# Kernel tuning notes

Measured on AMD Instinct MI355X. Metric: run time of the kernel, lower is better.

## Reference

```python
import jax, jax.numpy as jnp
import numpy as np

TOP_N = 2
NUM_GATES = 8
EPS = 1e-9
THRESHOLD = 0.2          # threshold_train for the 2nd expert
CAPACITY_FACTOR = 1.25   # capacity_factor_train (training mode)
MIN_EXPERT_CAPACITY = 4


def setup_inputs() -> dict:
    key = jax.random.key(0)
    k1, k2, k3 = jax.random.split(key, 3)
    b, n, dim = 4, 2048, 1024
    x = jax.random.normal(k1, (b, n, dim), jnp.float32)
    W_g = jax.random.normal(k2, (NUM_GATES, dim), jnp.float32) * 0.02
    # replaces torch.zeros_like(gates).uniform_(0,1) inside forward
    probs = jax.random.uniform(k3, (TOP_N, b, n), jnp.float32)
    return {"x": x, "W_g": W_g, "probs": probs}


def reference(x, W_g, probs):
    b, n, dim = x.shape
    expert_capacity = max(min(n, int(n * CAPACITY_FACTOR / NUM_GATES)), MIN_EXPERT_CAPACITY)
    cap_f = float(expert_capacity)

    gate_logits = jnp.einsum('bnd,ed->bne', x, W_g)            # [b,n,e]
    raw_gates = jax.nn.softmax(gate_logits, axis=-1)

    vals, idx = jax.lax.top_k(raw_gates, TOP_N)                # [b,n,k]
    gates = jnp.moveaxis(vals, -1, 0)                          # [k,b,n]
    gate_indices = jnp.moveaxis(idx, -1, 0)                    # [k,b,n]
    one_hot = jax.nn.one_hot(gate_indices, NUM_GATES, dtype=jnp.float32)  # [k,b,n,e]
    mask_1 = one_hot[0]                                        # taken before should_route masking

    denom = jnp.clip(gates.sum(axis=0, keepdims=True), EPS)
    gates = gates / denom                                      # renormalized top-n gates

    threshold = jnp.clip(jnp.array([EPS, THRESHOLD], jnp.float32), EPS)
    should_route = probs < gates / threshold[:, None, None]    # [k,b,n]
    should_route = should_route.at[0].set(True)
    mask = one_hot * should_route[..., None].astype(jnp.float32)

    # exclusive cumsum over the sequence (n) axis
    mask_cumsum = jnp.cumsum(mask, axis=2) - mask              # [k,b,n,e]

    prev_expert_count = jnp.zeros((b, 1, NUM_GATES), jnp.float32)
    masks, positions = [], []
    for t in range(TOP_N):
        pos = (mask_cumsum[t] + prev_expert_count) * mask[t]   # [b,n,e]
        m = mask[t] * (pos < cap_f).astype(jnp.float32)        # capacity drop
        prev_expert_count = prev_expert_count + m.sum(axis=1, keepdims=True)
        positions.append(pos.sum(axis=-1))                     # [b,n]
        masks.append(m)
    mask = jnp.stack(masks)                                    # [k,b,n,e]
    positions = jnp.stack(positions)                           # [k,b,n]

    mask_flat = mask.sum(axis=-1)                              # [k,b,n] in {0,1}
    gates = gates * mask_flat

    # one_hot over capacity; out-of-range positions (dropped tokens) -> all zeros,
    # matching safe_one_hot truncation
    pos_oh = jax.nn.one_hot(positions.astype(jnp.int32), expert_capacity, dtype=jnp.float32)  # [k,b,n,c]
    combine = jnp.einsum('kbn,kbn,kbne,kbnc->bnec', gates, mask_flat, one_hot, pos_oh)

    dispatch = (combine != 0).astype(x.dtype)
    dispatch = dispatch + combine - jax.lax.stop_gradient(combine)  # straight-through

    # training-mode aux losses
    density_1 = mask_1.mean(axis=1)                            # [b,e]
    density_1_proxy = raw_gates.mean(axis=1)                   # [b,e]
    balance_loss = (density_1_proxy * density_1).mean() * float(NUM_GATES ** 2)

    z = jax.nn.logsumexp(gate_logits, axis=-1)
    router_z_loss = jnp.mean(jnp.square(z))

    return dispatch, combine, balance_loss, router_z_loss
```

## Files before the change

kernel.cpp:

```cpp
#include <hip/hip_runtime.h>
#include <math.h>

#define BATCH 4
#define SEQ 2048
#define DIM 1024
#define NEXP 8
#define TOKENS (BATCH * SEQ)
#define CAP 320
#define C4 (CAP / 4)
#define DISP_ELEMS (TOKENS * NEXP * CAP)
#define FILL_F4 (DISP_ELEMS / 4)

struct alignas(16) Rec { float g0, g1; unsigned meta, pad; };

#define WS_GSUM_F 0
#define WS_CNT1_F 32
#define WS_Z2_F   64
#define WS_REC_B  1024
#define WS_POS0_B (WS_REC_B + 131072)
#define WS_POS1_B (WS_POS0_B + 32768)
#define WS_CNT0_B (WS_POS1_B + 32768)

__global__ __launch_bounds__(256) void gating_kernel(
    const float* __restrict__ x, const float* __restrict__ Wg,
    const float* __restrict__ probs, float* __restrict__ ws_f,
    Rec* __restrict__ recs)
{
    __shared__ float Wlds[NEXP * DIM];
    __shared__ float gsum_l[NEXP];
    __shared__ float cnt1_l[NEXP];
    __shared__ float z2_l;

    const int tid = threadIdx.x;
    float4* W4 = reinterpret_cast<float4*>(Wlds);
    const float4* Wg4 = reinterpret_cast<const float4*>(Wg);
    #pragma unroll
    for (int j = tid; j < NEXP * DIM / 4; j += 256) W4[j] = Wg4[j];
    if (tid < NEXP) { gsum_l[tid] = 0.f; cnt1_l[tid] = 0.f; }
    if (tid == 0) z2_l = 0.f;
    __syncthreads();

    const int wave = tid >> 6, lane = tid & 63;
    const int token0 = blockIdx.x * 16 + wave * 4;
    const int b = (blockIdx.x * 16) >> 11;

    float acc[4][NEXP];
    #pragma unroll
    for (int t = 0; t < 4; ++t)
        #pragma unroll
        for (int e = 0; e < NEXP; ++e) acc[t][e] = 0.f;

    const float4* x4 = reinterpret_cast<const float4*>(x);
    #pragma unroll
    for (int i = 0; i < 4; ++i) {
        const int j = lane + i * 64;
        float4 wv[NEXP];
        #pragma unroll
        for (int e = 0; e < NEXP; ++e) wv[e] = W4[e * 256 + j];
        #pragma unroll
        for (int t = 0; t < 4; ++t) {
            const float4 xv = x4[(size_t)(token0 + t) * 256 + j];
            #pragma unroll
            for (int e = 0; e < NEXP; ++e)
                acc[t][e] += xv.x * wv[e].x + xv.y * wv[e].y +
                             xv.z * wv[e].z + xv.w * wv[e].w;
        }
    }
    #pragma unroll
    for (int t = 0; t < 4; ++t)
        #pragma unroll
        for (int e = 0; e < NEXP; ++e) {
            float v = acc[t][e];
            #pragma unroll
            for (int o = 32; o > 0; o >>= 1) v += __shfl_xor(v, o, 64);
            acc[t][e] = v;
        }

    #pragma unroll
    for (int t = 0; t < 4; ++t) {
        const int token = token0 + t;
        float l[NEXP];
        #pragma unroll
        for (int e = 0; e < NEXP; ++e) l[e] = acc[t][e];
        float m = l[0];
        #pragma unroll
        for (int e = 1; e < NEXP; ++e) m = fmaxf(m, l[e]);
        float ex[NEXP], s = 0.f;
        #pragma unroll
        for (int e = 0; e < NEXP; ++e) { ex[e] = expf(l[e] - m); s += ex[e]; }
        const float inv = 1.f / s;
        int e0 = 0; float b0 = l[0];
        #pragma unroll
        for (int e = 1; e < NEXP; ++e) if (l[e] > b0) { b0 = l[e]; e0 = e; }
        int e1 = -1; float b1 = -1e30f;
        #pragma unroll
        for (int e = 0; e < NEXP; ++e)
            if (e != e0 && l[e] > b1) { b1 = l[e]; e1 = e; }
        const float v0 = ex[e0] * inv, v1 = ex[e1] * inv;
        float denom = v0 + v1; if (denom < 1e-9f) denom = 1e-9f;
        const float g0 = v0 / denom, g1 = v1 / denom;
        const float z = m + logf(s);
        const int route = (probs[TOKENS + token] < g1 / 0.2f) ? 1 : 0;
        if (lane == 0) {
            Rec r; r.g0 = g0; r.g1 = g1;
            r.meta = (unsigned)e0 | ((unsigned)e1 << 8) | ((unsigned)route << 16);
            r.pad = 0;
            recs[token] = r;
            #pragma unroll
            for (int e = 0; e < NEXP; ++e) atomicAdd(&gsum_l[e], ex[e] * inv);
            atomicAdd(&cnt1_l[e0], 1.0f);
            atomicAdd(&z2_l, z * z);
        }
    }
    __syncthreads();
    if (tid < NEXP) {
        atomicAdd(&ws_f[WS_GSUM_F + b * NEXP + tid], gsum_l[tid]);
        atomicAdd(&ws_f[WS_CNT1_F + b * NEXP + tid], cnt1_l[tid]);
    }
    if (tid == 0) atomicAdd(&ws_f[WS_Z2_F], z2_l);
}

__global__ __launch_bounds__(256) void scan_kernel(
    const Rec* __restrict__ recs, int* __restrict__ pos0,
    int* __restrict__ pos1, int* __restrict__ cnt0)
{
    const int blk = blockIdx.x;
    const int b = blk >> 3, e = blk & 7;
    const int tid = threadIdx.x;
    __shared__ unsigned lds[256];

    const int base_tok = b * SEQ + tid * 8;
    unsigned f0bits = 0, f1bits = 0;
    #pragma unroll
    for (int j = 0; j < 8; ++j) {
        const unsigned meta = recs[base_tok + j].meta;
        const int e0 = meta & 255, e1 = (meta >> 8) & 255, rt = (meta >> 16) & 1;
        if (e0 == e) f0bits |= 1u << j;
        if (e1 == e && rt) f1bits |= 1u << j;
    }
    const unsigned s0 = __popc(f0bits), s1 = __popc(f1bits);
    const unsigned v = s0 | (s1 << 16);
    lds[tid] = v;
    __syncthreads();
    for (int off = 1; off < 256; off <<= 1) {
        const unsigned t = (tid >= off) ? lds[tid - off] : 0u;
        __syncthreads();
        lds[tid] += t;
        __syncthreads();
    }
    const unsigned inc = lds[tid];
    const unsigned exc = inc - v;
    int p0 = (int)(exc & 0xffffu);
    int p1 = (int)(exc >> 16);
    #pragma unroll
    for (int j = 0; j < 8; ++j) {
        if (f0bits & (1u << j)) pos0[base_tok + j] = p0++;
        if (f1bits & (1u << j)) pos1[base_tok + j] = p1++;
    }
    if (tid == 255) cnt0[blk] = (int)(inc & 0xffffu);
}

__global__ __launch_bounds__(256) void fill_kernel(
    float* __restrict__ out, const Rec* __restrict__ recs,
    const int* __restrict__ pos0, const int* __restrict__ pos1,
    const int* __restrict__ cnt0, const float* __restrict__ ws_f)
{
    const unsigned fid = blockIdx.x * 256u + threadIdx.x;
    const unsigned c4 = fid % (unsigned)C4;
    const unsigned row = fid / (unsigned)C4;
    const unsigned e = row & 7u;
    const unsigned token = row >> 3;
    const unsigned b = token >> 11;

    const Rec r = recs[token];
    const unsigned e0 = r.meta & 255u;
    const unsigned e1 = (r.meta >> 8) & 255u;
    const unsigned rt = (r.meta >> 16) & 1u;

    const int cbase = (int)(c4 * 4u);
    int p = -1000;
    float g = 0.f;
    if (e0 == e) {
        p = pos0[token]; g = r.g0;
    } else if (e1 == e && rt) {
        int c0 = cnt0[b * NEXP + e]; if (c0 > CAP) c0 = CAP;
        const int pp = pos1[token] + c0;
        if (pp < CAP) { p = pp; g = r.g1; }
    }
    const int s = p - cbase;
    float4 comb, disp;
    comb.x = (s == 0) ? g : 0.f; disp.x = (s == 0) ? 1.f : 0.f;
    comb.y = (s == 1) ? g : 0.f; disp.y = (s == 1) ? 1.f : 0.f;
    comb.z = (s == 2) ? g : 0.f; disp.z = (s == 2) ? 1.f : 0.f;
    comb.w = (s == 3) ? g : 0.f; disp.w = (s == 3) ? 1.f : 0.f;

    float4* o4 = reinterpret_cast<float4*>(out);
    o4[fid] = disp;
    o4[fid + (unsigned)FILL_F4] = comb;

    if (fid == 0) {
        float bal = 0.f;
        #pragma unroll
        for (int i = 0; i < 32; ++i)
            bal += ws_f[WS_GSUM_F + i] * ws_f[WS_CNT1_F + i];
        bal *= 64.0f / (2048.0f * 2048.0f * 32.0f);
        const float rz = ws_f[WS_Z2_F] / (float)TOKENS;
        out[(size_t)2 * DISP_ELEMS]     = bal;
        out[(size_t)2 * DISP_ELEMS + 1] = rz;
    }
}

extern "C" void kernel_launch(void* const* d_in, const int* in_sizes, int n_in,
                              void* d_out, int out_size, void* d_ws, size_t ws_size,
                              hipStream_t stream) {
    const float* x     = (const float*)d_in[0];
    const float* Wg    = (const float*)d_in[1];
    const float* probs = (const float*)d_in[2];
    float* out = (float*)d_out;

    char* ws = (char*)d_ws;
    float* ws_f = (float*)ws;
    Rec*  recs  = (Rec*)(ws + WS_REC_B);
    int*  pos0  = (int*)(ws + WS_POS0_B);
    int*  pos1  = (int*)(ws + WS_POS1_B);
    int*  cnt0  = (int*)(ws + WS_CNT0_B);

    hipMemsetAsync(ws, 0, 512, stream);

    gating_kernel<<<TOKENS / 16, 256, 0, stream>>>(x, Wg, probs, ws_f, recs);
    scan_kernel<<<BATCH * NEXP, 256, 0, stream>>>(recs, pos0, pos1, cnt0);
    fill_kernel<<<FILL_F4 / 256, 256, 0, stream>>>(out, recs, pos0, pos1, cnt0, ws_f);
}
```

Baseline: 214.1 us.

## Split dense output fill into bulk zeroing plus sparse per-token scatter

The old fill kernel computed every float4 of the dispatch and combine tensors with per-element div/mod and a record lookup. It is replaced by a grid-stride zero kernel that writes only zeros, then a per-token scatter kernel that writes the at most two nonzero entries of dispatch and combine per token. This removes per-element index arithmetic and gather loads from the bandwidth-bound write of about 168 MB. In exchange it adds a kernel launch and a dependency between the zero and scatter passes.

```diff
diff --git a/kernel.cpp b/kernel.cpp
--- a/kernel.cpp
+++ b/kernel.cpp
@@ -7,9 +7,8 @@
 #define NEXP 8
 #define TOKENS (BATCH * SEQ)
 #define CAP 320
-#define C4 (CAP / 4)
 #define DISP_ELEMS (TOKENS * NEXP * CAP)
-#define FILL_F4 (DISP_ELEMS / 4)
+#define ZERO_F4 (2 * DISP_ELEMS / 4)
 
 struct alignas(16) Rec { float g0, g1; unsigned meta, pad; };
 
@@ -160,45 +159,44 @@
     if (tid == 255) cnt0[blk] = (int)(inc & 0xffffu);
 }
 
-__global__ __launch_bounds__(256) void fill_kernel(
+__global__ __launch_bounds__(256) void zero_kernel(float4* __restrict__ o4)
+{
+    const size_t stride = (size_t)gridDim.x * 256;
+    size_t i = (size_t)blockIdx.x * 256 + threadIdx.x;
+    const float4 z = make_float4(0.f, 0.f, 0.f, 0.f);
+    #pragma unroll 10
+    for (; i < (size_t)ZERO_F4; i += stride) o4[i] = z;
+}
+
+__global__ __launch_bounds__(256) void scatter_kernel(
     float* __restrict__ out, const Rec* __restrict__ recs,
     const int* __restrict__ pos0, const int* __restrict__ pos1,
     const int* __restrict__ cnt0, const float* __restrict__ ws_f)
 {
-    const unsigned fid = blockIdx.x * 256u + threadIdx.x;
-    const unsigned c4 = fid % (unsigned)C4;
-    const unsigned row = fid / (unsigned)C4;
-    const unsigned e = row & 7u;
-    const unsigned token = row >> 3;
-    const unsigned b = token >> 11;
-
+    const int token = blockIdx.x * 256 + threadIdx.x;
     const Rec r = recs[token];
-    const unsigned e0 = r.meta & 255u;
-    const unsigned e1 = (r.meta >> 8) & 255u;
-    const unsigned rt = (r.meta >> 16) & 1u;
-
-    const int cbase = (int)(c4 * 4u);
-    int p = -1000;
-    float g = 0.f;
-    if (e0 == e) {
-        p = pos0[token]; g = r.g0;
-    } else if (e1 == e && rt) {
-        int c0 = cnt0[b * NEXP + e]; if (c0 > CAP) c0 = CAP;
-        const int pp = pos1[token] + c0;
-        if (pp < CAP) { p = pp; g = r.g1; }
-    }
-    const int s = p - cbase;
-    float4 comb, disp;
-    comb.x = (s == 0) ? g : 0.f; disp.x = (s == 0) ? 1.f : 0.f;
-    comb.y = (s == 1) ? g : 0.f; disp.y = (s == 1) ? 1.f : 0.f;
-    comb.z = (s == 2) ? g : 0.f; disp.z = (s == 2) ? 1.f : 0.f;
-    comb.w = (s == 3) ? g : 0.f; disp.w = (s == 3) ? 1.f : 0.f;
-
-    float4* o4 = reinterpret_cast<float4*>(out);
-    o4[fid] = disp;
-    o4[fid + (unsigned)FILL_F4] = comb;
-
-    if (fid == 0) {
+    const int e0 = (int)(r.meta & 255u);
+    const int e1 = (int)((r.meta >> 8) & 255u);
+    const int rt = (int)((r.meta >> 16) & 1u);
+    const int b = token >> 11;
+
+    const int p0 = pos0[token];
+    if (p0 < CAP) {
+        const size_t idx = ((size_t)token * NEXP + e0) * CAP + p0;
+        out[idx] = 1.0f;
+        out[(size_t)DISP_ELEMS + idx] = r.g0;
+    }
+    if (rt) {
+        int c0 = cnt0[b * NEXP + e1]; if (c0 > CAP) c0 = CAP;
+        const int p1 = pos1[token] + c0;
+        if (p1 < CAP) {
+            const size_t idx = ((size_t)token * NEXP + e1) * CAP + p1;
+            out[idx] = 1.0f;
+            out[(size_t)DISP_ELEMS + idx] = r.g1;
+        }
+    }
+
+    if (token == 0) {
         float bal = 0.f;
         #pragma unroll
         for (int i = 0; i < 32; ++i)
@@ -229,5 +227,7 @@
 
     gating_kernel<<<TOKENS / 16, 256, 0, stream>>>(x, Wg, probs, ws_f, recs);
     scan_kernel<<<BATCH * NEXP, 256, 0, stream>>>(recs, pos0, pos1, cnt0);
-    fill_kernel<<<FILL_F4 / 256, 256, 0, stream>>>(out, recs, pos0, pos1, cnt0, ws_f);
-}
+    zero_kernel<<<4096, 256, 0, stream>>>(reinterpret_cast<float4*>(out));
+    scatter_kernel<<<TOKENS / 256, 256, 0, stream>>>(out, recs, pos0, pos1,
+                                                     cnt0, ws_f);
+}
```

Measured after the change: 219.3 us. 2.4% more time.
